# Kernel optimization log

Measured on AMD Instinct MI355X. Metric: run time of the kernel, lower is better.

## Reference

```python
import jax, jax.numpy as jnp
import numpy as np

N_NODES = 200000
DEG = 16
T = 3


def _w(key, shape, scale=0.05):
    return (jax.random.normal(key, shape, dtype=jnp.float32) * scale)


def setup_inputs() -> dict:
    key = jax.random.key(0)
    ks = jax.random.split(key, 24)
    inp = {
        'h': jax.random.normal(ks[0], (N_NODES, 70), dtype=jnp.float32),
        'edge_feats': jax.random.normal(ks[1], (N_NODES, DEG, 6), dtype=jnp.float32),
        'nbr_idx': jax.random.randint(ks[2], (N_NODES, DEG), 0, N_NODES, dtype=jnp.int32),
        # V: Linear(70,70) (shared across all T rounds, since ModuleList([m]*T) aliases)
        'Vw': _w(ks[3], (70, 70)), 'Vb': _w(ks[4], (70,)),
        # E: Linear(6,6)
        'Ew': _w(ks[5], (6, 6)), 'Eb': _w(ks[6], (6,)),
        # U: Linear(146,70) (shared across rounds)
        'Uw': _w(ks[7], (146, 70)), 'Ub': _w(ks[8], (70,)),
        # R: Linear(140,128)
        'Rw': _w(ks[9], (140, 128)), 'Rb': _w(ks[10], (128,)),
        # shared_hidden1: 128->128, shared_hidden2: 128->100
        'S1w': _w(ks[11], (128, 128)), 'S1b': _w(ks[12], (128,)),
        'S2w': _w(ks[13], (128, 100)), 'S2b': _w(ks[14], (100,)),
        # task head (n_tasks=1): hidden 100->100, output 100->1
        'Hw': _w(ks[15], (100, 100)), 'Hb': _w(ks[16], (100,)),
        'Ow': _w(ks[17], (100, 1)), 'Ob': _w(ks[18], (1,)),
    }
    return inp


def reference(h, edge_feats, nbr_idx, Vw, Vb, Ew, Eb, Uw, Ub, Rw, Rb,
              S1w, S1b, S2w, S2b, Hw, Hb, Ow, Ob):
    # Message passing: per neighbor slot j (sequential state update, as the
    # original updates h[v] in place per neighbor), applied to all nodes at once.
    xs = (jnp.transpose(nbr_idx), jnp.swapaxes(edge_feats, 0, 1))  # [DEG,N], [DEG,N,6]

    def step(hc, x):
        idx, e = x
        m_w = hc[idx] @ Vw + Vb                 # gather neighbor states, V(h[w])
        m_e = e @ Ew + Eb                       # E(e_vw)
        hc = jax.nn.relu(jnp.concatenate([hc, m_w, m_e], axis=1) @ Uw + Ub)
        return hc, None

    for _ in range(T):  # U/V are shared across rounds (ModuleList aliasing)
        h, _ = jax.lax.scan(step, h, xs)

    # Readout: h2 aliases h in the original torch code, so cat([h, h]) (dim 140)
    fm = jnp.sum(jax.nn.relu(jnp.concatenate([h, h], axis=1) @ Rw + Rb), axis=0)  # [128]
    a = jax.nn.relu(fm @ S1w + S1b)   # ReLU(ReLU(.)) == ReLU(.)
    b = a @ S2w + S2b                 # no activation before hidden layer
    c = jax.nn.relu(b @ Hw + Hb)
    out = c @ Ow + Ob                 # [1]
    return out[None, :]               # [n_tasks=1, 1]
```

## Files before the change

### kernel.cpp

```cpp
#include <hip/hip_runtime.h>
#include <hip/hip_bf16.h>


#define NNODES 200000
#define DEG 16

typedef __attribute__((ext_vector_type(8))) short short8;
typedef __attribute__((ext_vector_type(4))) float f32x4;

__device__ __forceinline__ unsigned short f2bf(float f) {
    unsigned u = __float_as_uint(f);
    unsigned r = 0x7FFFu + ((u >> 16) & 1u);
    return (unsigned short)((u + r) >> 16);
}

__global__ void prep_kernel(const float* __restrict__ Vw, const float* __restrict__ Vb,
                            const float* __restrict__ Ew, const float* __restrict__ Eb,
                            const float* __restrict__ Uw, const float* __restrict__ Ub,
                            const float* __restrict__ Rw,
                            float* __restrict__ Bstep, unsigned short* __restrict__ Btg,
                            float* __restrict__ bias80, unsigned short* __restrict__ Rcg) {
    const int t = threadIdx.x;
    for (int idx = t; idx < 70 * 70; idx += 256) Bstep[idx] = Uw[idx];
    for (int idx = t; idx < 70 * 70; idx += 256) {
        const int c = idx / 70, n = idx % 70;
        float s = 0.f;
        for (int c2 = 0; c2 < 70; ++c2) s += Vw[c * 70 + c2] * Uw[(70 + c2) * 70 + n];
        Bstep[(70 + c) * 70 + n] = s;
    }
    for (int idx = t; idx < 6 * 70; idx += 256) {
        const int c = idx / 70, n = idx % 70;
        float s = 0.f;
        for (int c2 = 0; c2 < 6; ++c2) s += Ew[c * 6 + c2] * Uw[(140 + c2) * 70 + n];
        Bstep[(140 + c) * 70 + n] = s;
    }
    __syncthreads();
    for (int idx = t; idx < 80 * 224; idx += 256) {
        const int n = idx / 224, k = idx % 224;
        float v = 0.f;
        if (n < 70) {
            if (k < 70) v = Bstep[k * 70 + n];
            else if (k >= 96 && k < 166) v = Bstep[(k - 26) * 70 + n];
            else if (k >= 192 && k < 198) v = Bstep[(k - 52) * 70 + n];
        }
        Btg[idx] = f2bf(v);
    }
    for (int n = t; n < 80; n += 256) {
        float s = 0.f;
        if (n < 70) {
            s = Ub[n];
            for (int c2 = 0; c2 < 70; ++c2) s += Vb[c2] * Uw[(70 + c2) * 70 + n];
            for (int c2 = 0; c2 < 6; ++c2) s += Eb[c2] * Uw[(140 + c2) * 70 + n];
        }
        bias80[n] = s;
    }
    for (int idx = t; idx < 128 * 96; idx += 256) {
        const int n = idx / 96, k = idx % 96;
        const float v = (k < 70) ? (Rw[k * 128 + n] + Rw[(70 + k) * 128 + n]) : 0.f;
        Rcg[idx] = f2bf(v);
    }
}

__global__ void conv_h_kernel(const float* __restrict__ h0, unsigned short* __restrict__ hb) {
    const long total = (long)NNODES * 36;
    for (long i = (long)blockIdx.x * blockDim.x + threadIdx.x; i < total;
         i += (long)gridDim.x * blockDim.x) {
        const long node = i / 36;
        const int kp = (int)(i % 36);
        unsigned v = 0u;
        if (kp < 35) {
            const float* p = h0 + node * 70 + kp * 2;
            v = (unsigned)f2bf(p[0]) | ((unsigned)f2bf(p[1]) << 16);
        }
        ((unsigned*)(hb + node * 72))[kp] = v;
    }
}

__global__ void conv_e_kernel(const float* __restrict__ e, unsigned short* __restrict__ eb) {
    const long total = (long)NNODES * DEG * 4;
    for (long i = (long)blockIdx.x * blockDim.x + threadIdx.x; i < total;
         i += (long)gridDim.x * blockDim.x) {
        const long row = i / 4;
        const int c = (int)(i % 4);
        unsigned v = 0u;
        if (c < 3) {
            const float* p = e + row * 6 + c * 2;
            v = (unsigned)f2bf(p[0]) | ((unsigned)f2bf(p[1]) << 16);
        }
        ((unsigned*)(eb + row * 8))[c] = v;
    }
}

__global__ __launch_bounds__(512) void step_kernel(
    const unsigned short* __restrict__ hin, const unsigned short* __restrict__ edgeb,
    const int* __restrict__ nbr, const unsigned short* __restrict__ Btg,
    const float* __restrict__ bias80, unsigned short* __restrict__ hout, const int j) {
    __shared__ __align__(16) unsigned short Btb[80 * 232];
    __shared__ float bias_s[80];
    const int tid = threadIdx.x;
    const long node0 = (long)blockIdx.x * 128;

    for (int i = tid; i < 80 * 112; i += 512) {
        const int n = i / 112, kp = i % 112;
        *(unsigned int*)&Btb[n * 232 + kp * 2] = ((const unsigned int*)Btg)[i];
    }
    if (tid < 80) bias_s[tid] = bias80[tid];

    const int w = tid >> 6, l = tid & 63;
    const int lm = l & 15, lhi = l >> 4, lk = lhi * 8;
    const long anode = node0 + w * 16 + lm;
    const long nl = anode < NNODES ? anode : (NNODES - 1);
    const int g = nbr[nl * DEG + j];

    short8 a[7];
    {
        const unsigned short* hr = hin + nl * 72;
        a[0] = *(const short8*)(hr + lk);
        a[1] = *(const short8*)(hr + 32 + lk);
        a[2] = *(const short8*)(hr + 64 + lk);
        const unsigned short* gr = hin + (long)g * 72;
        a[3] = *(const short8*)(gr + lk);
        a[4] = *(const short8*)(gr + 32 + lk);
        a[5] = *(const short8*)(gr + 64 + lk);
        a[6] = *(const short8*)(edgeb + (nl * DEG + j) * 8 + lk);
    }
    __syncthreads();

    f32x4 acc[5] = {{0.f, 0.f, 0.f, 0.f}, {0.f, 0.f, 0.f, 0.f}, {0.f, 0.f, 0.f, 0.f},
                    {0.f, 0.f, 0.f, 0.f}, {0.f, 0.f, 0.f, 0.f}};
#pragma unroll
    for (int kt = 0; kt < 7; ++kt) {
#pragma unroll
        for (int nt = 0; nt < 5; ++nt) {
            const short8 b = *(const short8*)&Btb[(nt * 16 + lm) * 232 + kt * 32 + lk];
            acc[nt] = __builtin_amdgcn_mfma_f32_16x16x32_bf16(a[kt], b, acc[nt], 0, 0, 0);
        }
    }

#pragma unroll
    for (int nt = 0; nt < 5; ++nt) {
        const int col = nt * 16 + lm;
        if (col < 70) {
            const float bias = bias_s[col];
#pragma unroll
            for (int r = 0; r < 4; ++r) {
                const long dnode = node0 + w * 16 + lhi * 4 + r;
                if (dnode < NNODES)
                    hout[dnode * 72 + col] = f2bf(fmaxf(acc[nt][r] + bias, 0.f));
            }
        }
    }
}

__global__ __launch_bounds__(512) void readout_kernel(
    const unsigned short* __restrict__ hb, const unsigned short* __restrict__ Rcg,
    const float* __restrict__ Rb, float* __restrict__ fm) {
    __shared__ __align__(16) unsigned short Rs[128 * 104];
    __shared__ float Rb_s[128];
    __shared__ float red[8][128];
    const int tid = threadIdx.x;
    const long node0 = (long)blockIdx.x * 128;

    for (int i = tid; i < 128 * 48; i += 512) {
        const int n = i / 48, kp = i % 48;
        *(unsigned int*)&Rs[n * 104 + kp * 2] = ((const unsigned int*)Rcg)[i];
    }
    if (tid < 128) Rb_s[tid] = Rb[tid];

    const int w = tid >> 6, l = tid & 63;
    const int lm = l & 15, lhi = l >> 4, lk = lhi * 8;
    const long anode = node0 + w * 16 + lm;
    const long nl = anode < NNODES ? anode : (NNODES - 1);
    short8 a[3];
    {
        const unsigned short* hr = hb + nl * 72;
        a[0] = *(const short8*)(hr + lk);
        a[1] = *(const short8*)(hr + 32 + lk);
        a[2] = *(const short8*)(hr + 64 + lk);
    }
    __syncthreads();

    f32x4 acc[8] = {{0.f, 0.f, 0.f, 0.f}, {0.f, 0.f, 0.f, 0.f}, {0.f, 0.f, 0.f, 0.f},
                    {0.f, 0.f, 0.f, 0.f}, {0.f, 0.f, 0.f, 0.f}, {0.f, 0.f, 0.f, 0.f},
                    {0.f, 0.f, 0.f, 0.f}, {0.f, 0.f, 0.f, 0.f}};
#pragma unroll
    for (int kt = 0; kt < 3; ++kt) {
#pragma unroll
        for (int nt = 0; nt < 8; ++nt) {
            const short8 b = *(const short8*)&Rs[(nt * 16 + lm) * 104 + kt * 32 + lk];
            acc[nt] = __builtin_amdgcn_mfma_f32_16x16x32_bf16(a[kt], b, acc[nt], 0, 0, 0);
        }
    }
#pragma unroll
    for (int nt = 0; nt < 8; ++nt) {
        const int col = nt * 16 + lm;
        const float bias = Rb_s[col];
        float s = 0.f;
#pragma unroll
        for (int r = 0; r < 4; ++r) {
            const long dnode = node0 + w * 16 + lhi * 4 + r;
            if (dnode < NNODES) s += fmaxf(acc[nt][r] + bias, 0.f);
        }
        s += __shfl_xor(s, 16);
        s += __shfl_xor(s, 32);
        if (l < 16) red[w][col] = s;
    }
    __syncthreads();
    if (tid < 128) {
        float s = 0.f;
#pragma unroll
        for (int r = 0; r < 8; ++r) s += red[r][tid];
        atomicAdd(&fm[tid], s);
    }
}

__global__ void mlp_kernel(const float* __restrict__ fm,
                           const float* __restrict__ S1w, const float* __restrict__ S1b,
                           const float* __restrict__ S2w, const float* __restrict__ S2b,
                           const float* __restrict__ Hw, const float* __restrict__ Hb,
                           const float* __restrict__ Ow, const float* __restrict__ Ob,
                           float* __restrict__ out) {
    __shared__ float fms[128], a_s[128], b_s[100], c_s[100];
    const int t = threadIdx.x;
    fms[t] = fm[t];
    __syncthreads();
    {
        float s = S1b[t];
        for (int c = 0; c < 128; ++c) s += fms[c] * S1w[c * 128 + t];
        a_s[t] = fmaxf(s, 0.f);
    }
    __syncthreads();
    if (t < 100) {
        float s = S2b[t];
        for (int c = 0; c < 128; ++c) s += a_s[c] * S2w[c * 100 + t];
        b_s[t] = s;
    }
    __syncthreads();
    if (t < 100) {
        float s = Hb[t];
        for (int c = 0; c < 100; ++c) s += b_s[c] * Hw[c * 100 + t];
        c_s[t] = fmaxf(s, 0.f);
    }
    __syncthreads();
    if (t == 0) {
        float s = Ob[0];
        for (int c = 0; c < 100; ++c) s += c_s[c] * Ow[c];
        out[0] = s;
    }
}

extern "C" void kernel_launch(void* const* d_in, const int* in_sizes, int n_in,
                              void* d_out, int out_size, void* d_ws, size_t ws_size,
                              hipStream_t stream) {
    const float* h0   = (const float*)d_in[0];
    const float* edge = (const float*)d_in[1];
    const int*   nbr  = (const int*)d_in[2];
    const float* Vw = (const float*)d_in[3];
    const float* Vb = (const float*)d_in[4];
    const float* Ew = (const float*)d_in[5];
    const float* Eb = (const float*)d_in[6];
    const float* Uw = (const float*)d_in[7];
    const float* Ub = (const float*)d_in[8];
    const float* Rw = (const float*)d_in[9];
    const float* Rb = (const float*)d_in[10];
    const float* S1w = (const float*)d_in[11];
    const float* S1b = (const float*)d_in[12];
    const float* S2w = (const float*)d_in[13];
    const float* S2b = (const float*)d_in[14];
    const float* Hw = (const float*)d_in[15];
    const float* Hb = (const float*)d_in[16];
    const float* Ow = (const float*)d_in[17];
    const float* Ob = (const float*)d_in[18];
    float* out = (float*)d_out;

    char* ws = (char*)d_ws;
    unsigned short* hA    = (unsigned short*)(ws);
    unsigned short* hB    = (unsigned short*)(ws + 28801024);
    unsigned short* edgeb = (unsigned short*)(ws + 57602048);
    unsigned short* Btg   = (unsigned short*)(ws + 108803072);
    unsigned short* Rcg   = (unsigned short*)(ws + 108838912);
    float* bias80 = (float*)(ws + 108863488);
    float* fm     = (float*)(ws + 108863808);
    float* Bstep  = (float*)(ws + 108864320);

    conv_h_kernel<<<2048, 256, 0, stream>>>(h0, hA);
    conv_e_kernel<<<2048, 256, 0, stream>>>(edge, edgeb);
    prep_kernel<<<1, 256, 0, stream>>>(Vw, Vb, Ew, Eb, Uw, Ub, Rw,
                                       Bstep, Btg, bias80, Rcg);
    hipMemsetAsync(fm, 0, 128 * sizeof(float), stream);

    const int nblk = (NNODES + 127) / 128;
    const unsigned short* cur = hA;
    for (int s = 0; s < 48; ++s) {
        unsigned short* o = (s & 1) ? hA : hB;
        step_kernel<<<nblk, 512, 0, stream>>>(cur, edgeb, nbr, Btg, bias80, o, s & 15);
        cur = o;
    }
    readout_kernel<<<nblk, 512, 0, stream>>>(cur, Rcg, Rb, fm);
    mlp_kernel<<<1, 128, 0, stream>>>(fm, S1w, S1b, S2w, S2b, Hw, Hb, Ow, Ob, out);
}
```

Measured before the change: 1.747 ms.

## Pre-swizzle MFMA B fragments and parallelize weight prep across blocks

Weight matrices are now stored in global memory already arranged in per-lane MFMA fragment order, so step and readout kernels copy them to LDS with 16-byte vector copies and read B operands contiguously by lane offset, avoiding padded row strides. The single-block prep kernel is split into two multi-block kernels so the one-time weight folding runs in parallel. Launch bounds now request 4 blocks per CU (512 threads each), which constrains register use in exchange for occupancy. LDS footprint also shrinks slightly.

```diff
diff --git a/kernel.cpp b/kernel.cpp
--- a/kernel.cpp
+++ b/kernel.cpp
@@ -14,50 +14,67 @@
     return (unsigned short)((u + r) >> 16);
 }
 
-__global__ void prep_kernel(const float* __restrict__ Vw, const float* __restrict__ Vb,
-                            const float* __restrict__ Ew, const float* __restrict__ Eb,
-                            const float* __restrict__ Uw, const float* __restrict__ Ub,
-                            const float* __restrict__ Rw,
-                            float* __restrict__ Bstep, unsigned short* __restrict__ Btg,
-                            float* __restrict__ bias80, unsigned short* __restrict__ Rcg) {
-    const int t = threadIdx.x;
-    for (int idx = t; idx < 70 * 70; idx += 256) Bstep[idx] = Uw[idx];
-    for (int idx = t; idx < 70 * 70; idx += 256) {
-        const int c = idx / 70, n = idx % 70;
-        float s = 0.f;
-        for (int c2 = 0; c2 < 70; ++c2) s += Vw[c * 70 + c2] * Uw[(70 + c2) * 70 + n];
-        Bstep[(70 + c) * 70 + n] = s;
-    }
-    for (int idx = t; idx < 6 * 70; idx += 256) {
-        const int c = idx / 70, n = idx % 70;
-        float s = 0.f;
-        for (int c2 = 0; c2 < 6; ++c2) s += Ew[c * 6 + c2] * Uw[(140 + c2) * 70 + n];
-        Bstep[(140 + c) * 70 + n] = s;
-    }
-    __syncthreads();
-    for (int idx = t; idx < 80 * 224; idx += 256) {
-        const int n = idx / 224, k = idx % 224;
-        float v = 0.f;
-        if (n < 70) {
-            if (k < 70) v = Bstep[k * 70 + n];
-            else if (k >= 96 && k < 166) v = Bstep[(k - 26) * 70 + n];
-            else if (k >= 192 && k < 198) v = Bstep[(k - 52) * 70 + n];
-        }
-        Btg[idx] = f2bf(v);
-    }
-    for (int n = t; n < 80; n += 256) {
-        float s = 0.f;
-        if (n < 70) {
-            s = Ub[n];
-            for (int c2 = 0; c2 < 70; ++c2) s += Vb[c2] * Uw[(70 + c2) * 70 + n];
-            for (int c2 = 0; c2 < 6; ++c2) s += Eb[c2] * Uw[(140 + c2) * 70 + n];
-        }
-        bias80[n] = s;
-    }
-    for (int idx = t; idx < 128 * 96; idx += 256) {
-        const int n = idx / 96, k = idx % 96;
-        const float v = (k < 70) ? (Rw[k * 128 + n] + Rw[(70 + k) * 128 + n]) : 0.f;
-        Rcg[idx] = f2bf(v);
+__device__ __forceinline__ int kmap(int k) {
+    if (k < 70) return k;
+    if (k >= 96 && k < 166) return k - 26;
+    if (k >= 192 && k < 198) return k - 52;
+    return -1;
+}
+
+__global__ void prepA_kernel(const float* __restrict__ Vw, const float* __restrict__ Vb,
+                             const float* __restrict__ Ew, const float* __restrict__ Eb,
+                             const float* __restrict__ Uw, const float* __restrict__ Ub,
+                             const float* __restrict__ Rw,
+                             float* __restrict__ Bstep, float* __restrict__ bias80,
+                             unsigned short* __restrict__ Rcg) {
+    const int b = blockIdx.x, t = threadIdx.x;
+    if (b < 70) {
+        if (t < 70) {
+            Bstep[b * 70 + t] = Uw[b * 70 + t];
+            float s = 0.f;
+            for (int c2 = 0; c2 < 70; ++c2) s += Vw[b * 70 + c2] * Uw[(70 + c2) * 70 + t];
+            Bstep[(70 + b) * 70 + t] = s;
+        }
+    } else if (b == 70) {
+        for (int i = t; i < 6 * 70; i += 256) {
+            const int c = i / 70, n = i % 70;
+            float s = 0.f;
+            for (int c2 = 0; c2 < 6; ++c2) s += Ew[c * 6 + c2] * Uw[(140 + c2) * 70 + n];
+            Bstep[(140 + c) * 70 + n] = s;
+        }
+    } else if (b == 71) {
+        if (t < 80) {
+            float s = 0.f;
+            if (t < 70) {
+                s = Ub[t];
+                for (int c2 = 0; c2 < 70; ++c2) s += Vb[c2] * Uw[(70 + c2) * 70 + t];
+                for (int c2 = 0; c2 < 6; ++c2) s += Eb[c2] * Uw[(140 + c2) * 70 + t];
+            }
+            bias80[t] = s;
+        }
+    } else {
+        const int f = b - 72;
+        const int nt = f & 7, kt = f >> 3;
+        for (int e = t; e < 512; e += 256) {
+            const int l = e >> 3, j = e & 7;
+            const int col = nt * 16 + (l & 15);
+            const int k = kt * 32 + (l >> 4) * 8 + j;
+            const float v = (k < 70) ? (Rw[k * 128 + col] + Rw[(70 + k) * 128 + col]) : 0.f;
+            Rcg[f * 512 + e] = f2bf(v);
+        }
+    }
+}
+
+__global__ void prepB_kernel(const float* __restrict__ Bstep, unsigned short* __restrict__ Btg) {
+    const int f = blockIdx.x, t = threadIdx.x;
+    const int nt = f % 5, kt = f / 5;
+    for (int e = t; e < 512; e += 256) {
+        const int l = e >> 3, j = e & 7;
+        const int col = nt * 16 + (l & 15);
+        const int k = kt * 32 + (l >> 4) * 8 + j;
+        const int kr = kmap(k);
+        const float v = (col < 70 && kr >= 0) ? Bstep[kr * 70 + col] : 0.f;
+        Btg[f * 512 + e] = f2bf(v);
     }
 }
 
@@ -91,23 +108,25 @@
     }
 }
 
-__global__ __launch_bounds__(512) void step_kernel(
+__global__ __launch_bounds__(512, 4) void step_kernel(
     const unsigned short* __restrict__ hin, const unsigned short* __restrict__ edgeb,
     const int* __restrict__ nbr, const unsigned short* __restrict__ Btg,
     const float* __restrict__ bias80, unsigned short* __restrict__ hout, const int j) {
-    __shared__ __align__(16) unsigned short Btb[80 * 232];
+    __shared__ __align__(16) unsigned short Btb[35 * 512];
     __shared__ float bias_s[80];
     const int tid = threadIdx.x;
     const long node0 = (long)blockIdx.x * 128;
 
-    for (int i = tid; i < 80 * 112; i += 512) {
-        const int n = i / 112, kp = i % 112;
-        *(unsigned int*)&Btb[n * 232 + kp * 2] = ((const unsigned int*)Btg)[i];
+    {
+        const uint4* src = (const uint4*)Btg;
+        uint4* dst = (uint4*)Btb;
+        for (int i = tid; i < 2240; i += 512) dst[i] = src[i];
     }
     if (tid < 80) bias_s[tid] = bias80[tid];
 
     const int w = tid >> 6, l = tid & 63;
     const int lm = l & 15, lhi = l >> 4, lk = lhi * 8;
+    const int lofs = l * 8;
     const long anode = node0 + w * 16 + lm;
     const long nl = anode < NNODES ? anode : (NNODES - 1);
     const int g = nbr[nl * DEG + j];
@@ -132,7 +151,7 @@
     for (int kt = 0; kt < 7; ++kt) {
 #pragma unroll
         for (int nt = 0; nt < 5; ++nt) {
-            const short8 b = *(const short8*)&Btb[(nt * 16 + lm) * 232 + kt * 32 + lk];
+            const short8 b = *(const short8*)&Btb[(kt * 5 + nt) * 512 + lofs];
             acc[nt] = __builtin_amdgcn_mfma_f32_16x16x32_bf16(a[kt], b, acc[nt], 0, 0, 0);
         }
     }
@@ -152,23 +171,25 @@
     }
 }
 
-__global__ __launch_bounds__(512) void readout_kernel(
+__global__ __launch_bounds__(512, 4) void readout_kernel(
     const unsigned short* __restrict__ hb, const unsigned short* __restrict__ Rcg,
     const float* __restrict__ Rb, float* __restrict__ fm) {
-    __shared__ __align__(16) unsigned short Rs[128 * 104];
+    __shared__ __align__(16) unsigned short Rs[24 * 512];
     __shared__ float Rb_s[128];
     __shared__ float red[8][128];
     const int tid = threadIdx.x;
     const long node0 = (long)blockIdx.x * 128;
 
-    for (int i = tid; i < 128 * 48; i += 512) {
-        const int n = i / 48, kp = i % 48;
-        *(unsigned int*)&Rs[n * 104 + kp * 2] = ((const unsigned int*)Rcg)[i];
+    {
+        const uint4* src = (const uint4*)Rcg;
+        uint4* dst = (uint4*)Rs;
+        for (int i = tid; i < 1536; i += 512) dst[i] = src[i];
     }
     if (tid < 128) Rb_s[tid] = Rb[tid];
 
     const int w = tid >> 6, l = tid & 63;
     const int lm = l & 15, lhi = l >> 4, lk = lhi * 8;
+    const int lofs = l * 8;
     const long anode = node0 + w * 16 + lm;
     const long nl = anode < NNODES ? anode : (NNODES - 1);
     short8 a[3];
@@ -187,7 +208,7 @@
     for (int kt = 0; kt < 3; ++kt) {
 #pragma unroll
         for (int nt = 0; nt < 8; ++nt) {
-            const short8 b = *(const short8*)&Rs[(nt * 16 + lm) * 104 + kt * 32 + lk];
+            const short8 b = *(const short8*)&Rs[(kt * 8 + nt) * 512 + lofs];
             acc[nt] = __builtin_amdgcn_mfma_f32_16x16x32_bf16(a[kt], b, acc[nt], 0, 0, 0);
         }
     }
@@ -285,8 +306,8 @@
 
     conv_h_kernel<<<2048, 256, 0, stream>>>(h0, hA);
     conv_e_kernel<<<2048, 256, 0, stream>>>(edge, edgeb);
-    prep_kernel<<<1, 256, 0, stream>>>(Vw, Vb, Ew, Eb, Uw, Ub, Rw,
-                                       Bstep, Btg, bias80, Rcg);
+    prepA_kernel<<<96, 256, 0, stream>>>(Vw, Vb, Ew, Eb, Uw, Ub, Rw, Bstep, bias80, Rcg);
+    prepB_kernel<<<35, 256, 0, stream>>>(Bstep, Btg);
     hipMemsetAsync(fm, 0, 128 * sizeof(float), stream);
 
     const int nblk = (NNODES + 127) / 128;
```

Result: faster. 1.665 ms (-4.7%).
